# Optimization experiments

Hardware: AMD Instinct MI355X
Metric: run time of the kernel (lower is better)

## Reference

```python
import jax, jax.numpy as jnp
import numpy as np

EPSILON = float(np.finfo(np.float32).eps)
EPS = 1e-05  # module eps (mask_norm=True)


def setup_inputs() -> dict:
    key = jax.random.key(0)
    ks = jax.random.split(key, 7)
    N, C, F, T = 8, 8, 257, 1000
    att_dim = 512
    return {
        "mask_s": jax.random.uniform(ks[0], (N, T, F), dtype=jnp.float32),
        "x_real": jax.random.normal(ks[1], (N, C, F, T), dtype=jnp.float32),
        "x_imag": jax.random.normal(ks[2], (N, C, F, T), dtype=jnp.float32),
        "proj_w": jax.random.normal(ks[3], (att_dim, F), dtype=jnp.float32) / np.sqrt(F),
        "proj_b": jax.random.normal(ks[4], (att_dim,), dtype=jnp.float32) * 0.01,
        "gvec_w": jax.random.normal(ks[5], (1, att_dim), dtype=jnp.float32) / np.sqrt(att_dim),
        "gvec_b": jax.random.normal(ks[6], (1,), dtype=jnp.float32) * 0.01,
    }


def _estimate_covar(mask, spec):
    # mask: N x F x T (real); spec: N x F x C x T (complex) -> covar N x F x C x C
    mm = mask[:, :, None, :]  # N F 1 T
    nom = jnp.einsum('nfit,nfjt->nfij', spec * mm, jnp.conj(spec))
    den = jnp.maximum(jnp.sum(mm, axis=-1, keepdims=True), EPSILON)  # N F 1 1
    return nom / den


def reference(mask_s, x_real, x_imag, proj_w, proj_b, gvec_w, gvec_b):
    x = jax.lax.complex(x_real, x_imag)  # N x C x F x T
    # _process_mask: inf-norm over time (dim=1 of N x T x F), then transpose -> N x F x T
    max_abs = jnp.max(jnp.abs(mask_s), axis=1, keepdims=True)
    ms = mask_s / (max_abs + EPSILON)
    ms = jnp.transpose(ms, (0, 2, 1))  # N F T
    mn = 1.0 - ms  # mask_n is None -> use 1 - processed speech mask

    spec = jnp.transpose(x, (0, 2, 1, 3))  # N F C T
    Rs = _estimate_covar(ms, spec)  # N F C C
    Rn = _estimate_covar(mn, spec)

    # ChannelAttention: u (N x C)
    C = Rs.shape[-1]
    I = jnp.eye(C, dtype=bool)
    Rs_off = jnp.where(I, 0.0, Rs).sum(-1) / (C - 1)  # N F C (complex)
    feat = jnp.transpose(jnp.abs(Rs_off), (0, 2, 1))  # N C F
    proj = jnp.tanh(feat @ proj_w.T + proj_b)  # N C att_dim
    g = (proj @ gvec_w.T + gvec_b)[..., 0]  # N C
    u = jax.nn.softmax(g, axis=-1)

    # MVDR weight: Rn^{-1} Rs u / tr(Rn^{-1} Rs)
    Rn = Rn + jnp.eye(C, dtype=Rn.dtype) * EPS
    Rn_inv = jnp.linalg.inv(Rn)  # N F C C
    RiRs = jnp.einsum('nfij,nfjk->nfik', Rn_inv, Rs)
    tr = jnp.trace(RiRs, axis1=-2, axis2=-1) + EPS  # N F
    w = jnp.einsum('nfic,nc->nfi', RiRs, u.astype(RiRs.dtype)) / tr[..., None]  # N F C
    w = jnp.transpose(w, (0, 2, 1))  # N C F

    # beamform: sum_c conj(w)[n,c,f] * x[n,c,f,t] -> N F T, then transpose -> N T F
    beam = jnp.sum(jnp.conj(w)[..., None] * x, axis=1)
    out = jnp.transpose(beam, (0, 2, 1))  # N T F complex
    return jnp.stack([out.real, out.imag], axis=-1)  # N T F 2 (real view)
```

## Files before the change

### kernel.cpp

```cpp
#include <hip/hip_runtime.h>
#include <hip/hip_bf16.h>
#include <cmath>

#define NB 8
#define CCH 8
#define FF 257
#define TT 1000
#define AD 512
#define EPSI 1.1920928955078125e-07f
#define EPS5 1e-05f
#define NCH 2
#define TCH 500

__host__ __device__ constexpr int PIDX(int i, int j) { return i * 8 - i * (i - 1) / 2 + (j - i); }
__host__ __device__ constexpr int QIDX(int i, int j) { return i * 7 - i * (i - 1) / 2 + (j - i - 1); }

__device__ constexpr int RI_[36] = {0,0,0,0,0,0,0,0, 1,1,1,1,1,1,1, 2,2,2,2,2,2, 3,3,3,3,3, 4,4,4,4, 5,5,5, 6,6, 7};
__device__ constexpr int RJ_[36] = {0,1,2,3,4,5,6,7, 1,2,3,4,5,6,7, 2,3,4,5,6,7, 3,4,5,6,7, 4,5,6,7, 5,6,7, 6,7, 7};
__device__ constexpr int QI_[28] = {0,0,0,0,0,0,0, 1,1,1,1,1,1, 2,2,2,2,2, 3,3,3,3, 4,4,4, 5,5, 6};
__device__ constexpr int QJ_[28] = {1,2,3,4,5,6,7, 2,3,4,5,6,7, 3,4,5,6,7, 4,5,6,7, 5,6,7, 6,7, 7};

#define REC_STRIDE 132

__device__ inline float wredsum(float v) {
#pragma unroll
    for (int o = 32; o; o >>= 1) v += __shfl_down(v, o, 64);
    return v;
}
__device__ inline float wredmax(float v) {
#pragma unroll
    for (int o = 32; o; o >>= 1) v = fmaxf(v, __shfl_down(v, o, 64));
    return v;
}

__global__ __launch_bounds__(64, 4) void cov_part_kernel(const float* __restrict__ mask,
                                                         const float* __restrict__ xr,
                                                         const float* __restrict__ xi,
                                                         float* __restrict__ cov) {
    const int kind = blockIdx.x;
    const int f = blockIdx.y;
    const int z = blockIdx.z;
    const int n = z >> 1, ch = z & 1;
    const int lane = threadIdx.x;
    const int t0 = ch * TCH;
    const bool isReal = (kind & 1) == 0;
    const bool isMasked = kind < 2;

    float acc[36] = {};
    float smask = 0.f, mmask = 0.f;

    const size_t cstride = (size_t)FF * TT;
    const float* xrb = xr + ((size_t)(n * CCH) * FF + f) * TT;
    const float* xib = xi + ((size_t)(n * CCH) * FF + f) * TT;
    const float* mb = mask + (size_t)n * TT * FF + f;

#pragma unroll
    for (int it = 0; it < 8; ++it) {
        const int tt = it * 64 + lane;
        if (tt < TCH) {
            const int t = t0 + tt;
            float w = 1.0f;
            if (isMasked) {
                float mv = mb[(size_t)t * FF];
                w = mv;
                if (kind == 0) { smask += mv; mmask = fmaxf(mmask, fabsf(mv)); }
            }
            float ar[8], ai[8];
#pragma unroll
            for (int c = 0; c < 8; c++) {
                ar[c] = xrb[c * cstride + t];
                ai[c] = xib[c * cstride + t];
            }
            if (isReal) {
#pragma unroll
                for (int e = 0; e < 36; e++)
                    acc[e] += w * (ar[RI_[e]] * ar[RJ_[e]] + ai[RI_[e]] * ai[RJ_[e]]);
            } else {
#pragma unroll
                for (int e = 0; e < 28; e++)
                    acc[e] += w * (ai[QI_[e]] * ar[QJ_[e]] - ar[QI_[e]] * ai[QJ_[e]]);
            }
        }
    }

    float* rec = cov + (size_t)(n * FF + f) * REC_STRIDE;
    const int base = (kind == 0) ? 0 : (kind == 1) ? 36 : (kind == 2) ? 64 : 100;
    if (isReal) {
#pragma unroll
        for (int e = 0; e < 36; e++) {
            float v = wredsum(acc[e]);
            if (lane == 0) atomicAdd(&rec[base + e], v);
        }
    } else {
#pragma unroll
        for (int e = 0; e < 28; e++) {
            float v = wredsum(acc[e]);
            if (lane == 0) atomicAdd(&rec[base + e], v);
        }
    }
    if (kind == 0) {
        float st = wredsum(smask);
        float mt = wredmax(mmask);
        if (lane == 0) {
            atomicAdd(&rec[128], st);
            atomicMax((int*)&rec[129], __float_as_int(mt));
        }
    }
}

__global__ __launch_bounds__(256) void attn_kernel(const float* __restrict__ cov,
                                                   const float* __restrict__ proj_w,
                                                   const float* __restrict__ proj_b,
                                                   const float* __restrict__ gvec_w,
                                                   float* __restrict__ gpart) {
    const int dc = blockIdx.x;
    const int n = blockIdx.y;
    const int tid = threadIdx.x;
    __shared__ float feat[8][FF];

    for (int f = tid; f < FF; f += 256) {
        const float* rec = cov + (size_t)(n * FF + f) * REC_STRIDE;
        float inv_mx = 1.0f / (rec[129] + EPSI);
        float sum_ms = rec[128] * inv_mx;
        float scale = inv_mx / (7.0f * fmaxf(sum_ms, EPSI));
#pragma unroll
        for (int i = 0; i < 8; i++) {
            float rr = 0.f, ri = 0.f;
#pragma unroll
            for (int j = 0; j < 8; j++) {
                if (j == i) continue;
                if (j > i) { rr += rec[PIDX(i, j)]; ri += rec[36 + QIDX(i, j)]; }
                else       { rr += rec[PIDX(j, i)]; ri -= rec[36 + QIDX(j, i)]; }
            }
            feat[i][f] = sqrtf(rr * rr + ri * ri) * scale;
        }
    }
    __syncthreads();

    const int wv = tid >> 6, lane = tid & 63;
    const int d = dc * 64 + lane;
    const int c0 = 2 * wv, c1 = c0 + 1;
    const float* pwd = proj_w + (size_t)d * FF;
    float a0 = proj_b[d], a1 = a0;
    for (int f = 0; f < FF; f++) {
        float w = pwd[f];
        a0 += w * feat[c0][f];
        a1 += w * feat[c1][f];
    }
    float gwd = gvec_w[d];
    float g0 = gwd * tanhf(a0);
    float g1 = gwd * tanhf(a1);
    g0 = wredsum(g0);
    g1 = wredsum(g1);
    if (!lane) {
        gpart[(n * 8 + dc) * 8 + c0] = g0;
        gpart[(n * 8 + dc) * 8 + c1] = g1;
    }
}

__global__ void attn2_kernel(const float* __restrict__ gpart, const float* __restrict__ gvec_b,
                             float* __restrict__ u) {
    const int n = blockIdx.x;
    const int lane = threadIdx.x;
    float v = gpart[n * 64 + lane];
    v += __shfl_xor(v, 8, 64);
    v += __shfl_xor(v, 16, 64);
    v += __shfl_xor(v, 32, 64);
    float g = v + gvec_b[0];
    float m = g;
    m = fmaxf(m, __shfl_xor(m, 1, 64));
    m = fmaxf(m, __shfl_xor(m, 2, 64));
    m = fmaxf(m, __shfl_xor(m, 4, 64));
    float e = expf(g - m);
    float s = e;
    s += __shfl_xor(s, 1, 64);
    s += __shfl_xor(s, 2, 64);
    s += __shfl_xor(s, 4, 64);
    if (lane < 8) u[n * 8 + lane] = e / s;
}

__global__ __launch_bounds__(64, 1) void solve_kernel(const float* __restrict__ cov,
                                                      const float* __restrict__ u,
                                                      float* __restrict__ wout) {
    const int idx = blockIdx.x * 64 + threadIdx.x;
    if (idx >= NB * FF) return;
    const int n = idx / FF;
    const float* rec = cov + (size_t)idx * REC_STRIDE;

    float raw = rec[128], mx = rec[129];
    float inv_mx = 1.0f / (mx + EPSI);
    float sum_ms = raw * inv_mx;
    float inv_s = 1.0f / fmaxf(sum_ms, EPSI);
    float inv_n = 1.0f / fmaxf((float)TT - sum_ms, EPSI);
    float ks = inv_mx * inv_s;

    float Ar[8][8], Ai[8][8], Br[8][8], Bi[8][8];
#pragma unroll
    for (int i = 0; i < 8; i++) {
#pragma unroll
        for (int j = i; j < 8; j++) {
            float mr = rec[PIDX(i, j)];
            float tr = rec[64 + PIDX(i, j)];
            float s_r = mr * ks;
            float n_r = (tr - mr * inv_mx) * inv_n;
            if (j == i) {
                Br[i][i] = s_r; Bi[i][i] = 0.f;
                Ar[i][i] = n_r + EPS5; Ai[i][i] = 0.f;
            } else {
                float mi = rec[36 + QIDX(i, j)];
                float ti = rec[100 + QIDX(i, j)];
                float s_i = mi * ks;
                float n_i = (ti - mi * inv_mx) * inv_n;
                Br[i][j] = s_r; Bi[i][j] = s_i;
                Br[j][i] = s_r; Bi[j][i] = -s_i;
                Ar[i][j] = n_r; Ai[i][j] = n_i;
                Ar[j][i] = n_r; Ai[j][i] = -n_i;
            }
        }
    }

#pragma unroll
    for (int k = 0; k < 8; k++) {
        float dr = Ar[k][k], di = Ai[k][k];
        float iv = 1.0f / (dr * dr + di * di);
        float pir = dr * iv, pii = -di * iv;
#pragma unroll
        for (int r = k + 1; r < 8; r++) {
            float ar = Ar[r][k], ai = Ai[r][k];
            float fr = ar * pir - ai * pii;
            float fi = ar * pii + ai * pir;
#pragma unroll
            for (int j = k + 1; j < 8; j++) {
                Ar[r][j] -= fr * Ar[k][j] - fi * Ai[k][j];
                Ai[r][j] -= fr * Ai[k][j] + fi * Ar[k][j];
            }
#pragma unroll
            for (int j = 0; j < 8; j++) {
                Br[r][j] -= fr * Br[k][j] - fi * Bi[k][j];
                Bi[r][j] -= fr * Bi[k][j] + fi * Br[k][j];
            }
        }
    }
#pragma unroll
    for (int k = 7; k >= 0; k--) {
        float dr = Ar[k][k], di = Ai[k][k];
        float iv = 1.0f / (dr * dr + di * di);
        float pir = dr * iv, pii = -di * iv;
#pragma unroll
        for (int j = 0; j < 8; j++) {
            float s_r = Br[k][j], s_i = Bi[k][j];
#pragma unroll
            for (int m = k + 1; m < 8; m++) {
                s_r -= Ar[k][m] * Br[m][j] - Ai[k][m] * Bi[m][j];
                s_i -= Ar[k][m] * Bi[m][j] + Ai[k][m] * Br[m][j];
            }
            Br[k][j] = s_r * pir - s_i * pii;
            Bi[k][j] = s_r * pii + s_i * pir;
        }
    }

    float trr = EPS5, tri = 0.f;
#pragma unroll
    for (int i = 0; i < 8; i++) { trr += Br[i][i]; tri += Bi[i][i]; }
    float tinv = 1.0f / (trr * trr + tri * tri);

    float* wo = wout + (size_t)idx * 16;
#pragma unroll
    for (int i = 0; i < 8; i++) {
        float nr = 0.f, ni = 0.f;
#pragma unroll
        for (int c = 0; c < 8; c++) {
            float uc = u[n * 8 + c];
            nr += Br[i][c] * uc;
            ni += Bi[i][c] * uc;
        }
        float wr = (nr * trr + ni * tri) * tinv;
        float wi = (ni * trr - nr * tri) * tinv;
        wo[i * 2] = wr;
        wo[i * 2 + 1] = -wi;
    }
}

__global__ __launch_bounds__(256) void beam_kernel(const float* __restrict__ xr,
                                                   const float* __restrict__ xi,
                                                   const float* __restrict__ wc,
                                                   float* __restrict__ out) {
    const int n = blockIdx.z;
    const int f0 = blockIdx.y * 32;
    const int t0 = blockIdx.x * 64;
    const int tid = threadIdx.x;

    __shared__ float wlds[32][16];
    __shared__ float bldr[32][65];
    __shared__ float bldi[32][65];

    for (int s = tid; s < 32 * 16; s += 256) {
        int fl = s >> 4, rest = s & 15;
        int f = f0 + fl;
        wlds[fl][rest] = (f < FF) ? wc[(size_t)(n * FF + f) * 16 + rest] : 0.f;
    }
    __syncthreads();

    const int lane_t = tid & 63, row = tid >> 6;
    const int t = t0 + lane_t;
    const bool tok = t < TT;
    const size_t cstride = (size_t)FF * TT;

#pragma unroll
    for (int k = 0; k < 8; k++) {
        int fl = row + k * 4;
        int f = f0 + fl;
        float br = 0.f, bi = 0.f;
        if (f < FF && tok) {
            size_t base = ((size_t)(n * CCH) * FF + f) * TT + t;
#pragma unroll
            for (int c = 0; c < 8; c++) {
                float vr = xr[base + c * cstride];
                float vi = xi[base + c * cstride];
                float wr = wlds[fl][c * 2], wi_ = wlds[fl][c * 2 + 1];
                br += wr * vr - wi_ * vi;
                bi += wr * vi + wi_ * vr;
            }
        }
        bldr[fl][lane_t] = br;
        bldi[fl][lane_t] = bi;
    }
    __syncthreads();

    const int fc = tid & 31, trb = tid >> 5;
    const int f = f0 + fc;
    float2* outv = (float2*)out;
#pragma unroll
    for (int k = 0; k < 8; k++) {
        int tr = trb + k * 8;
        int t2 = t0 + tr;
        if (f < FF && t2 < TT) {
            float2 v = make_float2(bldr[fc][tr], bldi[fc][tr]);
            outv[(size_t)(n * TT + t2) * FF + f] = v;
        }
    }
}

extern "C" void kernel_launch(void* const* d_in, const int* in_sizes, int n_in,
                              void* d_out, int out_size, void* d_ws, size_t ws_size,
                              hipStream_t stream) {
    const float* mask = (const float*)d_in[0];
    const float* xr = (const float*)d_in[1];
    const float* xi = (const float*)d_in[2];
    const float* pw = (const float*)d_in[3];
    const float* pb = (const float*)d_in[4];
    const float* gw = (const float*)d_in[5];
    const float* gb = (const float*)d_in[6];
    float* out = (float*)d_out;
    float* ws = (float*)d_ws;

    float* cov = ws;
    float* gpart = cov + (size_t)NB * FF * REC_STRIDE;
    float* u = gpart + 512;
    float* wv = u + 64;

    hipMemsetAsync(cov, 0, (size_t)NB * FF * REC_STRIDE * sizeof(float), stream);

    hipLaunchKernelGGL(cov_part_kernel, dim3(4, FF, NB * NCH), dim3(64), 0, stream, mask, xr, xi, cov);
    hipLaunchKernelGGL(attn_kernel, dim3(8, NB), dim3(256), 0, stream, cov, pw, pb, gw, gpart);
    hipLaunchKernelGGL(attn2_kernel, dim3(NB), dim3(64), 0, stream, gpart, gb, u);
    hipLaunchKernelGGL(solve_kernel, dim3((NB * FF + 63) / 64), dim3(64), 0, stream, cov, u, wv);
    hipLaunchKernelGGL(beam_kernel, dim3((TT + 63) / 64, (FF + 31) / 32, NB), dim3(256), 0, stream, xr, xi, wv, out);
}
```

Before: 228.6 us.

## Share staged channel tiles across four waves per frequency and pre-transpose mask

New measurement: 263.9 us. 15.4% more time.

```diff
diff --git a/kernel.cpp b/kernel.cpp
--- a/kernel.cpp
+++ b/kernel.cpp
@@ -9,8 +9,8 @@
 #define AD 512
 #define EPSI 1.1920928955078125e-07f
 #define EPS5 1e-05f
-#define NCH 2
-#define TCH 500
+#define TILE 256
+#define NTILE 4
 
 __host__ __device__ constexpr int PIDX(int i, int j) { return i * 8 - i * (i - 1) / 2 + (j - i); }
 __host__ __device__ constexpr int QIDX(int i, int j) { return i * 7 - i * (i - 1) / 2 + (j - i - 1); }
@@ -33,78 +33,131 @@
     return v;
 }
 
-__global__ __launch_bounds__(64, 4) void cov_part_kernel(const float* __restrict__ mask,
-                                                         const float* __restrict__ xr,
-                                                         const float* __restrict__ xi,
-                                                         float* __restrict__ cov) {
-    const int kind = blockIdx.x;
-    const int f = blockIdx.y;
-    const int z = blockIdx.z;
-    const int n = z >> 1, ch = z & 1;
-    const int lane = threadIdx.x;
-    const int t0 = ch * TCH;
-    const bool isReal = (kind & 1) == 0;
-    const bool isMasked = kind < 2;
-
-    float acc[36] = {};
-    float smask = 0.f, mmask = 0.f;
+__global__ __launch_bounds__(256) void mask_transpose_kernel(const float* __restrict__ mask,
+                                                             float* __restrict__ maskT) {
+    const int f0 = blockIdx.x * 32;
+    const int t0 = blockIdx.y * 32;
+    const int n = blockIdx.z;
+    const int tx = threadIdx.x & 31, ty = threadIdx.x >> 5;
+    __shared__ float tile[32][33];
+
+#pragma unroll
+    for (int k = 0; k < 4; k++) {
+        int t = t0 + ty + 8 * k, f = f0 + tx;
+        if (t < TT && f < FF) tile[ty + 8 * k][tx] = mask[((size_t)n * TT + t) * FF + f];
+    }
+    __syncthreads();
+#pragma unroll
+    for (int k = 0; k < 4; k++) {
+        int f = f0 + ty + 8 * k, t = t0 + tx;
+        if (f < FF && t < TT) maskT[((size_t)n * FF + f) * TT + t] = tile[tx][ty + 8 * k];
+    }
+}
+
+__global__ __launch_bounds__(256, 4) void cov_kernel(const float* __restrict__ maskT,
+                                                     const float* __restrict__ xr,
+                                                     const float* __restrict__ xi,
+                                                     float* __restrict__ cov) {
+    const int nf = blockIdx.x;
+    const int n = nf / FF, f = nf % FF;
+    const int wave = threadIdx.x >> 6, lane = threadIdx.x & 63;
+    const bool isReal = (wave & 1) == 0;
+    const bool isMasked = wave < 2;
+
+    __shared__ float lx[2][16][TILE];
 
     const size_t cstride = (size_t)FF * TT;
     const float* xrb = xr + ((size_t)(n * CCH) * FF + f) * TT;
     const float* xib = xi + ((size_t)(n * CCH) * FF + f) * TT;
-    const float* mb = mask + (size_t)n * TT * FF + f;
-
-#pragma unroll
-    for (int it = 0; it < 8; ++it) {
-        const int tt = it * 64 + lane;
-        if (tt < TCH) {
+    const float* mt = maskT + ((size_t)n * FF + f) * TT;
+
+    float acc[36] = {};
+    float smask = 0.f, mmask = 0.f;
+    float4 pre[4];
+
+    const int p0 = wave * 4;
+
+    auto load_regs = [&](int tile) {
+#pragma unroll
+        for (int p = 0; p < 4; p++) {
+            int pl = p0 + p, c = pl & 7;
+            int te = tile * TILE + lane * 4;
+            if (te < TT) {
+                const float* src = (pl < 8 ? xrb : xib) + c * cstride + te;
+                pre[p] = *(const float4*)src;
+            }
+        }
+    };
+    auto write_lds = [&](int b, int tile) {
+#pragma unroll
+        for (int p = 0; p < 4; p++) {
+            int te = tile * TILE + lane * 4;
+            if (te < TT) *(float4*)&lx[b][p0 + p][lane * 4] = pre[p];
+        }
+    };
+
+    load_regs(0);
+    write_lds(0, 0);
+    __syncthreads();
+
+    for (int tile = 0; tile < NTILE; ++tile) {
+        const int nxt = tile + 1;
+        if (nxt < NTILE) load_regs(nxt);
+
+        const int t0 = tile * TILE;
+        const int b = tile & 1;
+#pragma unroll
+        for (int sub = 0; sub < 4; sub++) {
+            const int tt = sub * 64 + lane;
             const int t = t0 + tt;
-            float w = 1.0f;
-            if (isMasked) {
-                float mv = mb[(size_t)t * FF];
-                w = mv;
-                if (kind == 0) { smask += mv; mmask = fmaxf(mmask, fabsf(mv)); }
-            }
-            float ar[8], ai[8];
-#pragma unroll
-            for (int c = 0; c < 8; c++) {
-                ar[c] = xrb[c * cstride + t];
-                ai[c] = xib[c * cstride + t];
-            }
-            if (isReal) {
-#pragma unroll
-                for (int e = 0; e < 36; e++)
-                    acc[e] += w * (ar[RI_[e]] * ar[RJ_[e]] + ai[RI_[e]] * ai[RJ_[e]]);
-            } else {
-#pragma unroll
-                for (int e = 0; e < 28; e++)
-                    acc[e] += w * (ai[QI_[e]] * ar[QJ_[e]] - ar[QI_[e]] * ai[QJ_[e]]);
-            }
-        }
-    }
-
-    float* rec = cov + (size_t)(n * FF + f) * REC_STRIDE;
-    const int base = (kind == 0) ? 0 : (kind == 1) ? 36 : (kind == 2) ? 64 : 100;
+            if (t < TT) {
+                float w = 1.0f;
+                if (isMasked) {
+                    float mv = mt[t];
+                    w = mv;
+                    if (wave == 0) { smask += mv; mmask = fmaxf(mmask, fabsf(mv)); }
+                }
+                float ar[8], ai[8];
+#pragma unroll
+                for (int c = 0; c < 8; c++) {
+                    ar[c] = lx[b][c][tt];
+                    ai[c] = lx[b][8 + c][tt];
+                }
+                if (isReal) {
+#pragma unroll
+                    for (int e = 0; e < 36; e++)
+                        acc[e] += w * (ar[RI_[e]] * ar[RJ_[e]] + ai[RI_[e]] * ai[RJ_[e]]);
+                } else {
+#pragma unroll
+                    for (int e = 0; e < 28; e++)
+                        acc[e] += w * (ai[QI_[e]] * ar[QJ_[e]] - ar[QI_[e]] * ai[QJ_[e]]);
+                }
+            }
+        }
+
+        if (nxt < NTILE) write_lds(nxt & 1, nxt);
+        __syncthreads();
+    }
+
+    float* rec = cov + (size_t)nf * REC_STRIDE;
+    const int base = (wave == 0) ? 0 : (wave == 1) ? 36 : (wave == 2) ? 64 : 100;
     if (isReal) {
 #pragma unroll
         for (int e = 0; e < 36; e++) {
             float v = wredsum(acc[e]);
-            if (lane == 0) atomicAdd(&rec[base + e], v);
+            if (lane == 0) rec[base + e] = v;
         }
     } else {
 #pragma unroll
         for (int e = 0; e < 28; e++) {
             float v = wredsum(acc[e]);
-            if (lane == 0) atomicAdd(&rec[base + e], v);
-        }
-    }
-    if (kind == 0) {
+            if (lane == 0) rec[base + e] = v;
+        }
+    }
+    if (wave == 0) {
         float st = wredsum(smask);
-        float mt = wredmax(mmask);
-        if (lane == 0) {
-            atomicAdd(&rec[128], st);
-            atomicMax((int*)&rec[129], __float_as_int(mt));
-        }
+        float mtx = wredmax(mmask);
+        if (lane == 0) { rec[128] = st; rec[129] = mtx; }
     }
 }
 
@@ -354,14 +407,14 @@
     float* out = (float*)d_out;
     float* ws = (float*)d_ws;
 
-    float* cov = ws;
+    float* maskT = ws;
+    float* cov = maskT + (size_t)NB * FF * TT;
     float* gpart = cov + (size_t)NB * FF * REC_STRIDE;
     float* u = gpart + 512;
     float* wv = u + 64;
 
-    hipMemsetAsync(cov, 0, (size_t)NB * FF * REC_STRIDE * sizeof(float), stream);
-
-    hipLaunchKernelGGL(cov_part_kernel, dim3(4, FF, NB * NCH), dim3(64), 0, stream, mask, xr, xi, cov);
+    hipLaunchKernelGGL(mask_transpose_kernel, dim3((FF + 31) / 32, (TT + 31) / 32, NB), dim3(256), 0, stream, mask, maskT);
+    hipLaunchKernelGGL(cov_kernel, dim3(NB * FF), dim3(256), 0, stream, maskT, xr, xi, cov);
     hipLaunchKernelGGL(attn_kernel, dim3(8, NB), dim3(256), 0, stream, cov, pw, pb, gw, gpart);
     hipLaunchKernelGGL(attn2_kernel, dim3(NB), dim3(64), 0, stream, gpart, gb, u);
     hipLaunchKernelGGL(solve_kernel, dim3((NB * FF + 63) / 64), dim3(64), 0, stream, cov, u, wv);
```

## Pre-transpose mask for coalesced loads and merge time chunks into one block

Applied to the files above, without the earlier changes.

Result: slower. 469.7 us (+105.5%).

```diff
diff --git a/kernel.cpp b/kernel.cpp
--- a/kernel.cpp
+++ b/kernel.cpp
@@ -9,7 +9,6 @@
 #define AD 512
 #define EPSI 1.1920928955078125e-07f
 #define EPS5 1e-05f
-#define NCH 2
 #define TCH 500
 
 __host__ __device__ constexpr int PIDX(int i, int j) { return i * 8 - i * (i - 1) / 2 + (j - i); }
@@ -33,15 +32,36 @@
     return v;
 }
 
-__global__ __launch_bounds__(64, 4) void cov_part_kernel(const float* __restrict__ mask,
-                                                         const float* __restrict__ xr,
-                                                         const float* __restrict__ xi,
-                                                         float* __restrict__ cov) {
+__global__ __launch_bounds__(256) void mask_transpose_kernel(const float* __restrict__ mask,
+                                                             float* __restrict__ maskT) {
+    const int f0 = blockIdx.x * 32;
+    const int t0 = blockIdx.y * 32;
+    const int n = blockIdx.z;
+    const int tx = threadIdx.x & 31, ty = threadIdx.x >> 5;
+    __shared__ float tile[32][33];
+
+#pragma unroll
+    for (int k = 0; k < 4; k++) {
+        int t = t0 + ty + 8 * k, f = f0 + tx;
+        if (t < TT && f < FF) tile[ty + 8 * k][tx] = mask[((size_t)n * TT + t) * FF + f];
+    }
+    __syncthreads();
+#pragma unroll
+    for (int k = 0; k < 4; k++) {
+        int f = f0 + ty + 8 * k, t = t0 + tx;
+        if (f < FF && t < TT) maskT[((size_t)n * FF + f) * TT + t] = tile[tx][ty + 8 * k];
+    }
+}
+
+__global__ __launch_bounds__(128, 4) void cov_part_kernel(const float* __restrict__ maskT,
+                                                          const float* __restrict__ xr,
+                                                          const float* __restrict__ xi,
+                                                          float* __restrict__ cov) {
     const int kind = blockIdx.x;
     const int f = blockIdx.y;
-    const int z = blockIdx.z;
-    const int n = z >> 1, ch = z & 1;
-    const int lane = threadIdx.x;
+    const int n = blockIdx.z;
+    const int ch = threadIdx.x >> 6;
+    const int lane = threadIdx.x & 63;
     const int t0 = ch * TCH;
     const bool isReal = (kind & 1) == 0;
     const bool isMasked = kind < 2;
@@ -52,7 +72,7 @@
     const size_t cstride = (size_t)FF * TT;
     const float* xrb = xr + ((size_t)(n * CCH) * FF + f) * TT;
     const float* xib = xi + ((size_t)(n * CCH) * FF + f) * TT;
-    const float* mb = mask + (size_t)n * TT * FF + f;
+    const float* mt = maskT + ((size_t)n * FF + f) * TT;
 
 #pragma unroll
     for (int it = 0; it < 8; ++it) {
@@ -61,7 +81,7 @@
             const int t = t0 + tt;
             float w = 1.0f;
             if (isMasked) {
-                float mv = mb[(size_t)t * FF];
+                float mv = mt[t];
                 w = mv;
                 if (kind == 0) { smask += mv; mmask = fmaxf(mmask, fabsf(mv)); }
             }
@@ -83,7 +103,7 @@
         }
     }
 
-    float* rec = cov + (size_t)(n * FF + f) * REC_STRIDE;
+    float* rec = cov + ((size_t)n * FF + f) * REC_STRIDE;
     const int base = (kind == 0) ? 0 : (kind == 1) ? 36 : (kind == 2) ? 64 : 100;
     if (isReal) {
 #pragma unroll
@@ -100,10 +120,10 @@
     }
     if (kind == 0) {
         float st = wredsum(smask);
-        float mt = wredmax(mmask);
+        float mtx = wredmax(mmask);
         if (lane == 0) {
             atomicAdd(&rec[128], st);
-            atomicMax((int*)&rec[129], __float_as_int(mt));
+            atomicMax((int*)&rec[129], __float_as_int(mtx));
         }
     }
 }
@@ -354,14 +374,16 @@
     float* out = (float*)d_out;
     float* ws = (float*)d_ws;
 
-    float* cov = ws;
+    float* maskT = ws;
+    float* cov = maskT + (size_t)NB * FF * TT;
     float* gpart = cov + (size_t)NB * FF * REC_STRIDE;
     float* u = gpart + 512;
     float* wv = u + 64;
 
     hipMemsetAsync(cov, 0, (size_t)NB * FF * REC_STRIDE * sizeof(float), stream);
 
-    hipLaunchKernelGGL(cov_part_kernel, dim3(4, FF, NB * NCH), dim3(64), 0, stream, mask, xr, xi, cov);
+    hipLaunchKernelGGL(mask_transpose_kernel, dim3((FF + 31) / 32, (TT + 31) / 32, NB), dim3(256), 0, stream, mask, maskT);
+    hipLaunchKernelGGL(cov_part_kernel, dim3(4, FF, NB), dim3(128), 0, stream, maskT, xr, xi, cov);
     hipLaunchKernelGGL(attn_kernel, dim3(8, NB), dim3(256), 0, stream, cov, pw, pb, gw, gpart);
     hipLaunchKernelGGL(attn2_kernel, dim3(NB), dim3(64), 0, stream, gpart, gb, u);
     hipLaunchKernelGGL(solve_kernel, dim3((NB * FF + 63) / 64), dim3(64), 0, stream, cov, u, wv);
```
